# Kernel optimization log

Hardware: AMD Instinct MI355X
Metric: run time of the kernel (lower is better)

Reference implementation:

```python
import jax, jax.numpy as jnp
import numpy as np

N_FZ, N_KEZ, N_TINT, N_ALPHA = 60, 20, 30, 200
NORB, NTIMES = 2000, 1000


def setup_inputs() -> dict:
    key = jax.random.key(0)
    k1, k2, k3, k4 = jax.random.split(key, 4)
    # log-spaced coordinate axes (as built in __init__ from fZs / alphas)
    log_fZs = jnp.linspace(-11.0, -9.0, N_FZ, dtype=jnp.float32)
    log_alphas = jnp.linspace(-2.0, 0.0, N_ALPHA, dtype=jnp.float32)
    alphas = 10.0 ** log_alphas
    kEZs = jnp.linspace(0.5, 10.0, N_KEZ, dtype=jnp.float32)  # sorted for searchsorted
    # grid already in stored layout (n_fZ, n_kEZ, n_tint, n_alpha)
    grid = 20.0 + 5.0 * jax.random.uniform(k1, (N_FZ, N_KEZ, N_TINT, N_ALPHA), dtype=jnp.float32)
    # angular separations, mostly inside [alphas[0], alphas[-1]] with some outside
    alpha = 10.0 ** jax.random.uniform(k2, (NORB, NTIMES), minval=-2.2, maxval=0.1, dtype=jnp.float32)
    dMag = 20.0 + 5.0 * jax.random.uniform(k3, (NORB, NTIMES), dtype=jnp.float32)
    fZ_vals = 10.0 ** jax.random.uniform(k4, (NTIMES,), minval=-11.0, maxval=-9.0, dtype=jnp.float32)
    kEZ_val = jnp.asarray(3.0, dtype=jnp.float32)
    return dict(alpha=alpha, dMag=dMag, fZ_vals=fZ_vals, kEZ_val=kEZ_val,
                grid=grid, kEZs=kEZs, alphas=alphas, log_fZs=log_fZs, log_alphas=log_alphas)


def reference(alpha, dMag, fZ_vals, kEZ_val, grid, kEZs, alphas, log_fZs, log_alphas):
    """Faithful translation of dMag0Grid._pdet_alpha_dMag.

    alpha, dMag : (norb, ntimes); fZ_vals : (ntimes,); kEZ_val : scalar.
    grid : (n_fZ, n_kEZ, n_tint, n_alpha).  Returns pdet : (ntimes, n_tint).
    """
    n_fZ = grid.shape[0]
    n_alpha = grid.shape[-1]
    inv_log_fZ_step = 1.0 / (log_fZs[1] - log_fZs[0])
    inv_log_alpha_step = 1.0 / (log_alphas[1] - log_alphas[0])

    geom_mask = (alpha >= alphas[0]) & (alpha <= alphas[-1])  # (norb, ntimes)

    # log-binned fZ index, per time
    fZ_ind = (jnp.log10(fZ_vals) - log_fZs[0]) * inv_log_fZ_step
    fZ0 = jnp.clip(jnp.floor(fZ_ind).astype(jnp.int32) + 1, 0, n_fZ - 2)  # (ntimes,)

    # log-binned alpha index, per (orbit, time)
    a_ind = (jnp.log10(alpha) - log_alphas[0]) * inv_log_alpha_step
    a0 = jnp.clip(a_ind.astype(jnp.int32), 0, n_alpha - 1)  # (norb, ntimes)
    dalpha = (a_ind - a0).astype(grid.dtype)

    kEZ_ind = jnp.searchsorted(kEZs, kEZ_val, side='right') - 1  # scalar

    # dynamic_slice clamps start so the size-2 window stays in bounds
    a0s = jnp.minimum(a0, n_alpha - 2)
    fZb = jnp.broadcast_to(fZ0[None, :], a0.shape)  # (norb, ntimes)

    sub = grid[:, kEZ_ind]          # (n_fZ, n_tint, n_alpha)
    g0 = sub[fZb, :, a0s]           # (norb, ntimes, n_tint) gather
    g1 = sub[fZb, :, a0s + 1]
    dim = g0 + dalpha[..., None] * (g1 - g0)  # linear interp in log-alpha

    det_mask = geom_mask[..., None] & jnp.signbit(dMag[..., None] - dim)
    pdet = det_mask.mean(axis=0)    # (ntimes, n_tint)
    return pdet
```

## Files before the change

### kernel.cpp

```cpp
#include <hip/hip_runtime.h>
#include <math.h>

#define N_FZ    60
#define N_KEZ   20
#define N_TINT  30
#define N_ALPHA 200
#define NORB    2000
#define NTIMES  1000
#define BLOCK   1024
#define P_LD    201

__global__ __launch_bounds__(256) void prep_kernel(
    const float* __restrict__ alpha,
    const float* __restrict__ dMag,
    const float* __restrict__ alphas,
    const float* __restrict__ log_alphas,
    float2* __restrict__ xd)
{
    __shared__ float2 tile[32][33];

    const float la0    = log_alphas[0];
    const float inv_la = 1.0f / (log_alphas[1] - la0);
    const float alo    = alphas[0];
    const float ahi    = alphas[N_ALPHA - 1];

    const int t0 = blockIdx.x * 32;
    const int o0 = blockIdx.y * 32;
    const int tx = threadIdx.x, ty = threadIdx.y;

    #pragma unroll
    for (int r = 0; r < 4; ++r) {
        int orb = o0 + ty + 8 * r;
        int t   = t0 + tx;
        float2 v = make_float2(0.0f, __builtin_inff());
        if (orb < NORB && t < NTIMES) {
            float a  = alpha[(size_t)orb * NTIMES + t];
            float dm = dMag [(size_t)orb * NTIMES + t];
            bool geom = (a >= alo) && (a <= ahi);
            float x = (log10f(a) - la0) * inv_la;
            float xc = fminf(fmaxf(x, 0.0f), 198.9999f);
            v = make_float2(xc, geom ? dm : __builtin_inff());
        }
        tile[ty + 8 * r][tx] = v;
    }
    __syncthreads();
    #pragma unroll
    for (int r = 0; r < 4; ++r) {
        int tt  = ty + 8 * r;
        int t   = t0 + tt;
        int orb = o0 + tx;
        if (orb < NORB && t < NTIMES)
            xd[(size_t)t * NORB + orb] = tile[tx][tt];
    }
}

__global__ __launch_bounds__(BLOCK) void pdet5_kernel(
    const float2* __restrict__ xd,
    const float* __restrict__ fZ_vals,
    const float* __restrict__ kEZ_val,
    const float* __restrict__ grid,
    const float* __restrict__ kEZs,
    const float* __restrict__ log_fZs,
    float* __restrict__ out)
{
    __shared__ float2 gs[N_TINT * P_LD];
    __shared__ int    wsum[16][N_TINT];

    const int t   = blockIdx.x;
    const int tid = threadIdx.x;

    const float lf0    = log_fZs[0];
    const float lfstep = log_fZs[1] - lf0;
    double fZ_ind = (log10((double)fZ_vals[t]) - (double)lf0) * (1.0 / (double)lfstep);
    int fZ0 = (int)floor(fZ_ind) + 1;
    fZ0 = min(max(fZ0, 0), N_FZ - 2);

    const float kv = kEZ_val[0];
    int kidx = -1;
    #pragma unroll
    for (int i = 0; i < N_KEZ; ++i) kidx += (kEZs[i] <= kv) ? 1 : 0;
    if (kidx < 0) kidx += N_KEZ;

    const float* src = grid + ((size_t)fZ0 * N_KEZ + kidx) * (N_TINT * N_ALPHA);
    for (int m = tid; m < N_TINT * 64; m += BLOCK) {
        int k = m >> 6;
        int c = m & 63;
        if (c < 50) {
            const float* p = src + (size_t)k * N_ALPHA + 4 * c;
            float4 v = *(const float4*)p;
            float nxt = p[4];
            int b = k * P_LD + 4 * c;
            gs[b + 0] = make_float2(v.x, v.y - v.x);
            gs[b + 1] = make_float2(v.y, v.z - v.y);
            gs[b + 2] = make_float2(v.z, v.w - v.z);
            gs[b + 3] = make_float2(v.w, nxt - v.w);
        }
    }
    __syncthreads();

    const int lane = tid & 63;
    const int w    = tid >> 6;
    const int s    = lane >> 5;
    const int k    = lane & 31;
    const int krow = min(k, N_TINT - 1) * P_LD;

    const float2* xp = xd + (size_t)t * NORB + 2 * w + s;

    int cnt = 0;
    #pragma unroll 9
    for (int i = 0; i < 62; ++i) {
        float2 v = xp[32 * i];
        unsigned a0 = (unsigned)v.x;
        float dal = __builtin_amdgcn_fractf(v.x);
        float2 p = gs[krow + a0];
        float dim = fmaf(dal, p.y, p.x);
        cnt += (v.y < dim) ? 1 : 0;
    }
    if (w < 8) {
        float2 v = xp[32 * 62];
        unsigned a0 = (unsigned)v.x;
        float dal = __builtin_amdgcn_fractf(v.x);
        float2 p = gs[krow + a0];
        float dim = fmaf(dal, p.y, p.x);
        cnt += (v.y < dim) ? 1 : 0;
    }

    cnt += __shfl_xor(cnt, 32, 64);
    if (s == 0 && k < N_TINT) wsum[w][k] = cnt;
    __syncthreads();

    if (tid < N_TINT) {
        int tot = 0;
        #pragma unroll
        for (int w2 = 0; w2 < 16; ++w2) tot += wsum[w2][tid];
        out[(size_t)t * N_TINT + tid] = (float)tot * (1.0f / NORB);
    }
}

__global__ __launch_bounds__(256) void pdet_kernel(
    const float* __restrict__ alpha, const float* __restrict__ dMag,
    const float* __restrict__ fZ_vals, const float* __restrict__ kEZ_val,
    const float* __restrict__ grid, const float* __restrict__ kEZs,
    const float* __restrict__ alphas, const float* __restrict__ log_fZs,
    const float* __restrict__ log_alphas, float* __restrict__ out)
{
    __shared__ float2 pairs[N_TINT * N_ALPHA];
    __shared__ int    wsum[4][N_TINT];

    const int t   = blockIdx.x;
    const int tid = threadIdx.x;

    const float la0    = log_alphas[0];
    const float inv_la = 1.0f / (log_alphas[1] - la0);
    const float alo    = alphas[0];
    const float ahi    = alphas[N_ALPHA - 1];

    const float lf0    = log_fZs[0];
    const float lfstep = log_fZs[1] - lf0;
    double fZ_ind = (log10((double)fZ_vals[t]) - (double)lf0) * (1.0 / (double)lfstep);
    int fZ0 = (int)floor(fZ_ind) + 1;
    fZ0 = min(max(fZ0, 0), N_FZ - 2);

    const float kv = kEZ_val[0];
    int kidx = -1;
    #pragma unroll
    for (int i = 0; i < N_KEZ; ++i) kidx += (kEZs[i] <= kv) ? 1 : 0;
    if (kidx < 0) kidx += N_KEZ;

    const float* src = grid + ((size_t)fZ0 * N_KEZ + kidx) * (N_TINT * N_ALPHA);
    const float4* src4 = (const float4*)src;
    for (int j = tid; j < (N_TINT * N_ALPHA) / 4; j += 256) {
        float4 v  = src4[j];
        float nxt = src[4 * j + 4];
        pairs[4 * j + 0] = make_float2(v.x, v.y);
        pairs[4 * j + 1] = make_float2(v.y, v.z);
        pairs[4 * j + 2] = make_float2(v.z, v.w);
        pairs[4 * j + 3] = make_float2(v.w, nxt);
    }
    __syncthreads();

    int cnt[N_TINT];
    #pragma unroll
    for (int k = 0; k < N_TINT; ++k) cnt[k] = 0;

    for (int orb = tid; orb < NORB; orb += 256) {
        float a  = alpha[(size_t)orb * NTIMES + t];
        float dm = dMag [(size_t)orb * NTIMES + t];
        bool geom = (a >= alo) && (a <= ahi);
        float a_ind = (log10f(a) - la0) * inv_la;
        int a0 = (int)a_ind;
        a0 = min(max(a0, 0), N_ALPHA - 1);
        float dal = a_ind - (float)a0;
        int a0s = min(a0, N_ALPHA - 2);
        if (!geom) dm = __builtin_inff();

        #pragma unroll
        for (int k = 0; k < N_TINT; ++k) {
            float2 p = pairs[k * N_ALPHA + a0s];
            float dim = p.x + dal * (p.y - p.x);
            cnt[k] += (dm < dim) ? 1 : 0;
        }
    }

    const int lane = tid & 63;
    const int wid  = tid >> 6;
    #pragma unroll
    for (int k = 0; k < N_TINT; ++k) {
        int c = cnt[k];
        c += __shfl_xor(c, 32, 64);
        c += __shfl_xor(c, 16, 64);
        c += __shfl_xor(c,  8, 64);
        c += __shfl_xor(c,  4, 64);
        c += __shfl_xor(c,  2, 64);
        c += __shfl_xor(c,  1, 64);
        if (lane == 0) wsum[wid][k] = c;
    }
    __syncthreads();

    if (tid < N_TINT) {
        int tot = wsum[0][tid] + wsum[1][tid] + wsum[2][tid] + wsum[3][tid];
        out[(size_t)t * N_TINT + tid] = (float)tot / (float)NORB;
    }
}

extern "C" void kernel_launch(void* const* d_in, const int* in_sizes, int n_in,
                              void* d_out, int out_size, void* d_ws, size_t ws_size,
                              hipStream_t stream) {
    const float* alpha      = (const float*)d_in[0];
    const float* dMag       = (const float*)d_in[1];
    const float* fZ_vals    = (const float*)d_in[2];
    const float* kEZ_val    = (const float*)d_in[3];
    const float* grid       = (const float*)d_in[4];
    const float* kEZs       = (const float*)d_in[5];
    const float* alphas     = (const float*)d_in[6];
    const float* log_fZs    = (const float*)d_in[7];
    const float* log_alphas = (const float*)d_in[8];
    float* out = (float*)d_out;

    const size_t need = (size_t)NTIMES * NORB * sizeof(float2);
    if (ws_size >= need) {
        dim3 gb((NTIMES + 31) / 32, (NORB + 31) / 32);
        dim3 tb(32, 8);
        prep_kernel<<<gb, tb, 0, stream>>>(alpha, dMag, alphas, log_alphas,
                                           (float2*)d_ws);
        pdet5_kernel<<<NTIMES, BLOCK, 0, stream>>>(
            (const float2*)d_ws, fZ_vals, kEZ_val, grid, kEZs, log_fZs, out);
    } else {
        pdet_kernel<<<NTIMES, 256, 0, stream>>>(
            alpha, dMag, fZ_vals, kEZ_val, grid, kEZs, alphas, log_fZs,
            log_alphas, out);
    }
}
```

Before: 128.9 us.

## Transpose shared grid table to alpha-major and load two tint pairs per float4

The main kernel now stores the interpolation table in shared memory as alpha-major rows holding all tint values, padded to 34 pairs. Each lane handles two tint columns through one 16-byte LDS read, and 16 lanes share one orbit's alpha index. This halves the number of LDS reads and the per-orbit global loads per count, at the cost of a strided, scalar table fill and duplicated work in the 16th lane. The fallback kernel also gets a padded, scalar pair-build loop, though it only runs when the workspace is too small.

After: 119.9 us. 1.08x faster.

```diff
diff --git a/kernel.cpp b/kernel.cpp
--- a/kernel.cpp
+++ b/kernel.cpp
@@ -8,7 +8,8 @@
 #define NORB    2000
 #define NTIMES  1000
 #define BLOCK   1024
-#define P_LD    201
+#define PAIR_LD 34
+#define N_ROWS  199
 
 __global__ __launch_bounds__(256) void prep_kernel(
     const float* __restrict__ alpha,
@@ -54,7 +55,7 @@
     }
 }
 
-__global__ __launch_bounds__(BLOCK) void pdet5_kernel(
+__global__ __launch_bounds__(BLOCK) void pdet6_kernel(
     const float2* __restrict__ xd,
     const float* __restrict__ fZ_vals,
     const float* __restrict__ kEZ_val,
@@ -63,8 +64,8 @@
     const float* __restrict__ log_fZs,
     float* __restrict__ out)
 {
-    __shared__ float2 gs[N_TINT * P_LD];
-    __shared__ int    wsum[16][N_TINT];
+    __shared__ __align__(16) float2 gsT[N_ROWS * PAIR_LD];
+    __shared__ int wsum[16][N_TINT];
 
     const int t   = blockIdx.x;
     const int tid = threadIdx.x;
@@ -82,51 +83,55 @@
     if (kidx < 0) kidx += N_KEZ;
 
     const float* src = grid + ((size_t)fZ0 * N_KEZ + kidx) * (N_TINT * N_ALPHA);
-    for (int m = tid; m < N_TINT * 64; m += BLOCK) {
-        int k = m >> 6;
-        int c = m & 63;
-        if (c < 50) {
-            const float* p = src + (size_t)k * N_ALPHA + 4 * c;
-            float4 v = *(const float4*)p;
-            float nxt = p[4];
-            int b = k * P_LD + 4 * c;
-            gs[b + 0] = make_float2(v.x, v.y - v.x);
-            gs[b + 1] = make_float2(v.y, v.z - v.y);
-            gs[b + 2] = make_float2(v.z, v.w - v.z);
-            gs[b + 3] = make_float2(v.w, nxt - v.w);
+    for (int m = tid; m < N_TINT * 256; m += BLOCK) {
+        int k = m >> 8;
+        int a = m & 255;
+        if (a < N_ROWS) {
+            const float* p = src + (size_t)k * N_ALPHA + a;
+            float g0 = p[0];
+            float g1 = p[1];
+            gsT[a * PAIR_LD + k] = make_float2(g0, g1 - g0);
         }
     }
     __syncthreads();
 
     const int lane = tid & 63;
     const int w    = tid >> 6;
-    const int s    = lane >> 5;
-    const int k    = lane & 31;
-    const int krow = min(k, N_TINT - 1) * P_LD;
-
-    const float2* xp = xd + (size_t)t * NORB + 2 * w + s;
-
-    int cnt = 0;
-    #pragma unroll 9
-    for (int i = 0; i < 62; ++i) {
-        float2 v = xp[32 * i];
+    const int s    = lane >> 4;
+    const int h    = lane & 15;
+    const int hh   = (h < 15) ? h : 14;
+
+    const float2* row = xd + (size_t)t * NORB;
+
+    int cnt_e = 0, cnt_o = 0;
+    #pragma unroll 8
+    for (int i = 0; i < 31; ++i) {
+        int q = w + 16 * i;
+        float2 v = row[4 * q + s];
         unsigned a0 = (unsigned)v.x;
         float dal = __builtin_amdgcn_fractf(v.x);
-        float2 p = gs[krow + a0];
-        float dim = fmaf(dal, p.y, p.x);
-        cnt += (v.y < dim) ? 1 : 0;
-    }
-    if (w < 8) {
-        float2 v = xp[32 * 62];
+        float4 P = *reinterpret_cast<const float4*>(&gsT[a0 * PAIR_LD + 2 * hh]);
+        cnt_e += (v.y < fmaf(dal, P.y, P.x)) ? 1 : 0;
+        cnt_o += (v.y < fmaf(dal, P.w, P.z)) ? 1 : 0;
+    }
+    if (w < 4) {
+        int q = 496 + w;
+        float2 v = row[4 * q + s];
         unsigned a0 = (unsigned)v.x;
         float dal = __builtin_amdgcn_fractf(v.x);
-        float2 p = gs[krow + a0];
-        float dim = fmaf(dal, p.y, p.x);
-        cnt += (v.y < dim) ? 1 : 0;
-    }
-
-    cnt += __shfl_xor(cnt, 32, 64);
-    if (s == 0 && k < N_TINT) wsum[w][k] = cnt;
+        float4 P = *reinterpret_cast<const float4*>(&gsT[a0 * PAIR_LD + 2 * hh]);
+        cnt_e += (v.y < fmaf(dal, P.y, P.x)) ? 1 : 0;
+        cnt_o += (v.y < fmaf(dal, P.w, P.z)) ? 1 : 0;
+    }
+
+    cnt_e += __shfl_xor(cnt_e, 16, 64);
+    cnt_e += __shfl_xor(cnt_e, 32, 64);
+    cnt_o += __shfl_xor(cnt_o, 16, 64);
+    cnt_o += __shfl_xor(cnt_o, 32, 64);
+    if (lane < 15) {
+        wsum[w][2 * lane]     = cnt_e;
+        wsum[w][2 * lane + 1] = cnt_o;
+    }
     __syncthreads();
 
     if (tid < N_TINT) {
@@ -144,7 +149,7 @@
     const float* __restrict__ alphas, const float* __restrict__ log_fZs,
     const float* __restrict__ log_alphas, float* __restrict__ out)
 {
-    __shared__ float2 pairs[N_TINT * N_ALPHA];
+    __shared__ float2 pairs[N_TINT * (N_ALPHA + 1)];
     __shared__ int    wsum[4][N_TINT];
 
     const int t   = blockIdx.x;
@@ -168,14 +173,12 @@
     if (kidx < 0) kidx += N_KEZ;
 
     const float* src = grid + ((size_t)fZ0 * N_KEZ + kidx) * (N_TINT * N_ALPHA);
-    const float4* src4 = (const float4*)src;
-    for (int j = tid; j < (N_TINT * N_ALPHA) / 4; j += 256) {
-        float4 v  = src4[j];
-        float nxt = src[4 * j + 4];
-        pairs[4 * j + 0] = make_float2(v.x, v.y);
-        pairs[4 * j + 1] = make_float2(v.y, v.z);
-        pairs[4 * j + 2] = make_float2(v.z, v.w);
-        pairs[4 * j + 3] = make_float2(v.w, nxt);
+    for (int j = tid; j < N_TINT * N_ALPHA; j += 256) {
+        int k = j / N_ALPHA;
+        int a = j - k * N_ALPHA;
+        float g0 = src[j];
+        float g1 = (a < N_ALPHA - 1) ? src[j + 1] : g0;
+        pairs[k * (N_ALPHA + 1) + a] = make_float2(g0, g1);
     }
     __syncthreads();
 
@@ -196,7 +199,7 @@
 
         #pragma unroll
         for (int k = 0; k < N_TINT; ++k) {
-            float2 p = pairs[k * N_ALPHA + a0s];
+            float2 p = pairs[k * (N_ALPHA + 1) + a0s];
             float dim = p.x + dal * (p.y - p.x);
             cnt[k] += (dm < dim) ? 1 : 0;
         }
@@ -243,7 +246,7 @@
         dim3 tb(32, 8);
         prep_kernel<<<gb, tb, 0, stream>>>(alpha, dMag, alphas, log_alphas,
                                            (float2*)d_ws);
-        pdet5_kernel<<<NTIMES, BLOCK, 0, stream>>>(
+        pdet6_kernel<<<NTIMES, BLOCK, 0, stream>>>(
             (const float2*)d_ws, fZ_vals, kEZ_val, grid, kEZs, log_fZs, out);
     } else {
         pdet_kernel<<<NTIMES, 256, 0, stream>>>(
```
